# Optimization experiments

Measured on AMD Instinct MI355X. Metric: run time of the kernel, lower is better.

The kernel has to match this reference:

```python
import jax, jax.numpy as jnp
import numpy as np

N_ITERS = 10
OMEGA = 10
W_HALF = 512          # hpm.W
D = 2 * W_HALF        # real-lifted signal dim
BATCH = 4096
P_PREV = 8
EPS = 1e-8


def hard_thr(x, omega=OMEGA):
    # x: [B, D]; keep the omega largest-|x| entries per row, zero the rest
    # (equivalent to torch scatter-zero of the D-omega smallest |x|)
    _, idx = jax.lax.top_k(jnp.abs(x), omega)            # [B, omega]
    rows = jnp.arange(x.shape[0])[:, None]
    mask = jnp.zeros_like(x).at[rows, idx].set(1.0)
    return x * mask


def _spectral_density(z):
    # z: [B, D] -> squared complex magnitude summed over batch, min-max normalized
    w = z.shape[1] // 2
    p = z[:, :w] ** 2 + z[:, w:] ** 2                    # [B, W] (sign flip of imag part cancels)
    mD = p.sum(0)                                        # [W]
    return (mD - mD.min()) / (mD.max() - mD.min() + EPS)


def setup_inputs() -> dict:
    key = jax.random.key(0)
    k0, k1, k2 = jax.random.split(key, 3)
    x = jax.random.normal(k0, (BATCH, D), jnp.float32)
    prev_windows = jax.random.normal(k1, (P_PREV, BATCH, D), jnp.float32)
    # learned dictionary (stand-in for the real-lifted partial Fourier matrix)
    W_d = jax.random.normal(k2, (1, D, D), jnp.float32) / np.sqrt(D).astype(np.float32)
    L = jnp.float32(5.0)                                 # hpm.L (fixed Lipschitz constant)
    S = jnp.eye(D, dtype=jnp.float32)[None] - (1.0 / L) * jnp.matmul(
        jnp.swapaxes(W_d, 1, 2), W_d)                    # [1, D, D]
    lambda2 = jnp.float32(1.0)
    return {"x": x, "prev_windows": prev_windows, "W_d": W_d, "S": S,
            "lambda2": lambda2, "L": L}


def reference(x, prev_windows, W_d, S, lambda2, L):
    Wd0 = W_d[0]                                         # [D, D]
    S0 = S[0]                                            # [D, D]
    w = D // 2

    # B = (1/L * W_d) @ x   (column-vector matvec as row GEMM)
    b = (x @ Wd0.T) / L                                  # [B, D]

    # two warm-up ISTA/IHT steps
    z = hard_thr(b)
    c = b + z @ S0.T
    z = hard_thr(c)

    mD_normalized = _spectral_density(z)                 # [W]

    # ---- attention over previous windows (prev_windows non-empty branch) ----
    pw = prev_windows                                    # [P, B, D]
    p_prev = pw[:, :, :w] ** 2 + pw[:, :, w:] ** 2       # [P, B, W]
    mD_prev = p_prev.sum(1)                              # [P, W]
    mn = mD_prev.min(axis=1, keepdims=True)
    mx = mD_prev.max(axis=1, keepdims=True)
    prev_mDn = (mD_prev - mn) / (mx - mn + EPS)          # [P, W]

    att = prev_mDn @ mD_normalized[:, None]              # [P, 1]
    att = jax.nn.softmax(att / np.sqrt(float(w)).astype(np.float32), axis=0)
    pw_clamped = jnp.clip(pw, -150.0, 150.0)
    z = (pw_clamped * att[:, None]).sum(0) * lambda2     # [B, D]

    # ---- unrolled iterations ----
    for _ in range(N_ITERS):
        c = b + z @ S0.T
        z = hard_thr(c)

    mD_normalized = _spectral_density(z)                 # [W]
    return (mD_normalized, z)
```

## Files before the change

kernel.cpp:

```cpp
#include <hip/hip_runtime.h>
#include <stdint.h>

#define BATCH 4096
#define DIM   1024
#define PPREV 8

__device__ __forceinline__ int wave_max_i32(int v) {
    #pragma unroll
    for (int m = 1; m < 64; m <<= 1) v = max(v, __shfl_xor(v, m));
    return v;
}
__device__ __forceinline__ int wave_min_i32(int v) {
    #pragma unroll
    for (int m = 1; m < 64; m <<= 1) v = min(v, __shfl_xor(v, m));
    return v;
}
__device__ __forceinline__ int lt_count(unsigned long long m) {
    return __builtin_amdgcn_mbcnt_hi((unsigned)(m >> 32),
           __builtin_amdgcn_mbcnt_lo((unsigned)m, 0));
}


__device__ __forceinline__ void top10_full(const int kin[16], int sgn, int lane,
                                           int wi[10], float wv[10]) {
    int k[16];
    #pragma unroll
    for (int s = 0; s < 16; ++s) k[s] = kin[s];
    #pragma unroll
    for (int r = 0; r < 10; ++r) {
        int lm = k[0]; int ls = 0;
        #pragma unroll
        for (int s = 1; s < 16; ++s) { if (k[s] > lm) { lm = k[s]; ls = s; } }
        int m = wave_max_i32(lm);
        int cj = (lm == m) ? ((lane << 4) | ls) : 4096;
        int jw = wave_min_i32(cj);
        int wl = jw >> 4, ws = jw & 15;
        int sg = __shfl(sgn, wl);
        wi[r] = jw;
        wv[r] = __int_as_float(m | (((sg >> ws) & 1) << 31));
        if (lane == wl) {
            #pragma unroll
            for (int s = 0; s < 16; ++s) if (s == ws) k[s] = 0;
        }
    }
}

template<bool SEEDED>
__device__ __forceinline__ void select10(const float cz[16], int lane,
                                         int* s_kb, int* s_pay,
                                         int& tbits, int wi[10], float wv[10]) {
    int k[16]; int sgn = 0;
    #pragma unroll
    for (int s = 0; s < 16; ++s) {
        int bb = __float_as_int(cz[s]);
        k[s] = bb & 0x7fffffff;
        sgn |= (int)(((unsigned)bb >> 31) << s);
    }

    if (!SEEDED) {
        int lm = k[0];
        #pragma unroll
        for (int s = 1; s < 16; ++s) lm = max(lm, k[s]);
        #pragma unroll
        for (int k2 = 2; k2 <= 64; k2 <<= 1) {
            #pragma unroll
            for (int j = k2 >> 1; j > 0; j >>= 1) {
                int p = __shfl_xor(lm, j);
                bool keep_max = (((lane & k2) == 0) == ((lane & j) == 0));
                if ((p > lm) == keep_max) lm = p;
            }
        }
        tbits = __builtin_amdgcn_readlane(lm, 9);
    }

    int tb = tbits;
    int total;
    #pragma unroll 1
    for (;;) {
        total = 0;
        #pragma unroll
        for (int s = 0; s < 16; ++s)
            total += __popcll(__ballot(k[s] >= tb));
        if (total >= 10) break;
        tb = (tb > 0x00800000) ? (tb - 0x00800000) : 0;
    }

    if (total <= 64) {
        int base = 0;
        #pragma unroll
        for (int s = 0; s < 16; ++s) {
            unsigned long long bs = __ballot(k[s] >= tb);
            if (k[s] >= tb) {
                int pos = base + lt_count(bs);
                s_kb[pos]  = k[s];
                s_pay[pos] = ((1023 - ((lane << 4) | s)) << 1) | ((sgn >> s) & 1);
            }
            base += __popcll(bs);
        }
        asm volatile("s_waitcnt lgkmcnt(0)" ::: "memory");
        int kb = -1, pay = 0;
        if (lane < total) { kb = s_kb[lane]; pay = s_pay[lane]; }
        #pragma unroll
        for (int k2 = 2; k2 <= 64; k2 <<= 1) {
            #pragma unroll
            for (int j = k2 >> 1; j > 0; j >>= 1) {
                int pk = __shfl_xor(kb, j);
                int pp = __shfl_xor(pay, j);
                bool keep_max = (((lane & k2) == 0) == ((lane & j) == 0));
                bool gt = (pk > kb) || ((pk == kb) && (pp > pay));
                if (gt == keep_max) { kb = pk; pay = pp; }
            }
        }
        #pragma unroll
        for (int r = 0; r < 10; ++r) {
            int kr = __builtin_amdgcn_readlane(kb, r);
            int pr = __builtin_amdgcn_readlane(pay, r);
            wi[r] = 1023 - (pr >> 1);
            wv[r] = __int_as_float(kr | ((pr & 1) << 31));
        }
        tbits = __builtin_amdgcn_readlane(kb, 9);
    } else {
        top10_full(k, sgn, lane, wi, wv);
        tbits = __float_as_int(wv[9]) & 0x7fffffff;
    }
}

__device__ __forceinline__ void gather_ista(const float bz[16], float cz[16],
                                            const float* __restrict__ S,
                                            const int wi[10], const float wv[10], int lane) {
    #pragma unroll
    for (int s = 0; s < 16; ++s) cz[s] = bz[s];
    #pragma unroll
    for (int kk = 0; kk < 10; ++kk) {
        const float4* sp = (const float4*)(S + (size_t)wi[kk] * DIM + (lane << 4));
        const float wvs = wv[kk];
        #pragma unroll
        for (int q = 0; q < 4; ++q) {
            float4 v = sp[q];
            cz[q*4+0] += wvs * v.x;
            cz[q*4+1] += wvs * v.y;
            cz[q*4+2] += wvs * v.z;
            cz[q*4+3] += wvs * v.w;
        }
    }
}

__global__ __launch_bounds__(64)
void warmup_rows(const float* __restrict__ b, const float* __restrict__ S,
                 int* __restrict__ sidx, float* __restrict__ sval) {
    __shared__ int s_kb[64];
    __shared__ int s_pay[64];
    const int lane = threadIdx.x;
    const int r = blockIdx.x;
    const float* bp = b + (size_t)r * DIM + (lane << 4);
    float bz[16];
    #pragma unroll
    for (int q = 0; q < 4; ++q) {
        float4 v = ((const float4*)bp)[q];
        bz[q*4+0] = v.x; bz[q*4+1] = v.y; bz[q*4+2] = v.z; bz[q*4+3] = v.w;
    }
    int wi[10]; float wv[10]; int tbits = 0;
    select10<false>(bz, lane, s_kb, s_pay, tbits, wi, wv);
    float cz[16];
    gather_ista(bz, cz, S, wi, wv, lane);
    select10<true>(cz, lane, s_kb, s_pay, tbits, wi, wv);
    if (lane == 0) {
        #pragma unroll
        for (int kk = 0; kk < 10; ++kk) { sidx[r*10+kk] = wi[kk]; sval[r*10+kk] = wv[kk]; }
    }
}

__global__ __launch_bounds__(64)
void loop_rows(const float* __restrict__ c1, const float* __restrict__ b,
               const float* __restrict__ S, float* __restrict__ zout,
               int* __restrict__ sidx, float* __restrict__ sval) {
    __shared__ int s_kb[64];
    __shared__ int s_pay[64];
    const int lane = threadIdx.x;
    const int r = blockIdx.x;
    const float* bp = b  + (size_t)r * DIM + (lane << 4);
    const float* cp = c1 + (size_t)r * DIM + (lane << 4);
    float bz[16], cz[16];
    #pragma unroll
    for (int q = 0; q < 4; ++q) {
        float4 v = ((const float4*)bp)[q];
        bz[q*4+0] = v.x; bz[q*4+1] = v.y; bz[q*4+2] = v.z; bz[q*4+3] = v.w;
        float4 u = ((const float4*)cp)[q];
        cz[q*4+0] = u.x; cz[q*4+1] = u.y; cz[q*4+2] = u.z; cz[q*4+3] = u.w;
    }
    int wi[10]; float wv[10]; int tbits = 0;
    select10<false>(cz, lane, s_kb, s_pay, tbits, wi, wv);
    int pwi[10], pwb[10];
    #pragma unroll 1
    for (int it = 0; it < 9; ++it) {
        #pragma unroll
        for (int kk = 0; kk < 10; ++kk) { pwi[kk] = wi[kk]; pwb[kk] = __float_as_int(wv[kk]); }
        gather_ista(bz, cz, S, wi, wv, lane);
        select10<true>(cz, lane, s_kb, s_pay, tbits, wi, wv);
        bool same = true;
        #pragma unroll
        for (int kk = 0; kk < 10; ++kk)
            same = same && (wi[kk] == pwi[kk]) && (__float_as_int(wv[kk]) == pwb[kk]);
        if (same) break;
    }
    #pragma unroll
    for (int q = 0; q < 4; ++q) {
        float e[4];
        #pragma unroll
        for (int t = 0; t < 4; ++t) {
            int j = (lane << 4) | (q*4 + t);
            float v = 0.0f;
            #pragma unroll
            for (int kk = 0; kk < 10; ++kk) v = (wi[kk] == j) ? wv[kk] : v;
            e[t] = v;
        }
        float4 o; o.x = e[0]; o.y = e[1]; o.z = e[2]; o.w = e[3];
        ((float4*)(zout + (size_t)r * DIM + (lane << 4)))[q] = o;
    }
    if (lane == 0) {
        #pragma unroll
        for (int kk = 0; kk < 10; ++kk) { sidx[r*10+kk] = wi[kk]; sval[r*10+kk] = wv[kk]; }
    }
}

template<bool DIV_L, bool HAS_ADD>
__global__ __launch_bounds__(512)
void gemm128(const float* __restrict__ A, const float* __restrict__ B,
             const float* __restrict__ addM, float* __restrict__ C,
             const float* __restrict__ Lptr, int M, int N, int K) {
    __shared__ float As[16][132];
    __shared__ float Bs[16][132];
    const int tid = threadIdx.x;
    const int m0 = blockIdx.y * 128, n0 = blockIdx.x * 128;
    const int tx = tid & 15;
    const int ty = tid >> 4;
    const int srow = tid >> 2;
    const int sk   = (tid & 3) * 4;
    float acc[4][8] = {};
    const float* Ab = A + (size_t)(m0 + srow) * K + sk;
    const float* Bb = B + (size_t)(n0 + srow) * K + sk;
    for (int k0 = 0; k0 < K; k0 += 16) {
        float4 av = *(const float4*)(Ab + k0);
        float4 bv = *(const float4*)(Bb + k0);
        __syncthreads();
        As[sk+0][srow] = av.x; As[sk+1][srow] = av.y; As[sk+2][srow] = av.z; As[sk+3][srow] = av.w;
        Bs[sk+0][srow] = bv.x; Bs[sk+1][srow] = bv.y; Bs[sk+2][srow] = bv.z; Bs[sk+3][srow] = bv.w;
        __syncthreads();
        #pragma unroll
        for (int k = 0; k < 16; ++k) {
            float4 a4  = *(const float4*)&As[k][ty*4];
            float4 b40 = *(const float4*)&Bs[k][tx*8];
            float4 b41 = *(const float4*)&Bs[k][tx*8+4];
            float am[4] = {a4.x, a4.y, a4.z, a4.w};
            float bn[8] = {b40.x, b40.y, b40.z, b40.w, b41.x, b41.y, b41.z, b41.w};
            #pragma unroll
            for (int i = 0; i < 4; ++i)
                #pragma unroll
                for (int j = 0; j < 8; ++j)
                    acc[i][j] += am[i] * bn[j];
        }
    }
    const float invL = DIV_L ? (1.0f / *Lptr) : 1.0f;
    #pragma unroll
    for (int i = 0; i < 4; ++i) {
        size_t row = (size_t)(m0 + ty*4 + i);
        float* Cp = C + row * N + n0 + tx*8;
        #pragma unroll
        for (int j = 0; j < 8; ++j) {
            float r = acc[i][j];
            if (DIV_L) r *= invL;
            if (HAS_ADD) r += addM[row * N + n0 + tx*8 + j];
            Cp[j] = r;
        }
    }
}

__global__ void sparse_density_stage1(const int* __restrict__ sidx,
                                      const float* __restrict__ sval,
                                      float* __restrict__ partial) {
    const int w = threadIdx.x;
    const int blk = blockIdx.x;
    const int base = blk * 64 * 10;
    float acc = 0.0f;
    for (int e = 0; e < 640; ++e) {
        int d = sidx[base + e];
        float v = sval[base + e];
        if ((d & 511) == w) acc += v * v;
    }
    partial[blk * 512 + w] = acc;
}

__global__ void density_stage2(const float* __restrict__ partial, float* __restrict__ mD) {
    const int w = threadIdx.x;
    float acc = 0.0f;
    for (int i = 0; i < 64; ++i) acc += partial[i * 512 + w];
    mD[w] = acc;
}

__global__ void prev_density_stage1(const float* __restrict__ pw, float* __restrict__ partial) {
    const int p = blockIdx.x, chunk = blockIdx.y;
    const int w = threadIdx.x;
    const float* base = pw + ((size_t)p * BATCH + (size_t)chunk * 64) * DIM;
    float acc = 0.0f;
    for (int i = 0; i < 64; ++i) {
        float a = base[(size_t)i * DIM + w];
        float c = base[(size_t)i * DIM + 512 + w];
        acc += a * a + c * c;
    }
    partial[((size_t)(p * 64 + chunk)) * 512 + w] = acc;
}

__global__ void prev_density_stage2(const float* __restrict__ partial, float* __restrict__ mD_prev) {
    const int p = blockIdx.x; const int w = threadIdx.x;
    float acc = 0.0f;
    for (int i = 0; i < 64; ++i) acc += partial[((size_t)(p * 64 + i)) * 512 + w];
    mD_prev[p * 512 + w] = acc;
}

__device__ __forceinline__ float wave_fmax(float v) {
    #pragma unroll
    for (int m = 1; m < 64; m <<= 1) v = fmaxf(v, __shfl_xor(v, m));
    return v;
}
__device__ __forceinline__ float wave_fmin(float v) {
    #pragma unroll
    for (int m = 1; m < 64; m <<= 1) v = fminf(v, __shfl_xor(v, m));
    return v;
}
__device__ __forceinline__ float wave_fsum(float v) {
    #pragma unroll
    for (int m = 1; m < 64; m <<= 1) v += __shfl_xor(v, m);
    return v;
}

__global__ void attention_small(const float* __restrict__ mD1,
                                const float* __restrict__ mD_prev,
                                float* __restrict__ att) {
    __shared__ float att_l[PPREV];
    const int tid = threadIdx.x, lane = tid & 63, w = tid >> 6;
    float t8[8], u8[8];
    {
        const float4* m4 = (const float4*)(mD1 + lane * 8);
        float4 a = m4[0], bq = m4[1];
        t8[0]=a.x; t8[1]=a.y; t8[2]=a.z; t8[3]=a.w; t8[4]=bq.x; t8[5]=bq.y; t8[6]=bq.z; t8[7]=bq.w;
        const float4* p4 = (const float4*)(mD_prev + w * 512 + lane * 8);
        float4 c = p4[0], d = p4[1];
        u8[0]=c.x; u8[1]=c.y; u8[2]=c.z; u8[3]=c.w; u8[4]=d.x; u8[5]=d.y; u8[6]=d.z; u8[7]=d.w;
    }
    float mx = t8[0], mn = t8[0], pmx = u8[0], pmn = u8[0];
    #pragma unroll
    for (int i = 1; i < 8; ++i) {
        mx = fmaxf(mx, t8[i]); mn = fminf(mn, t8[i]);
        pmx = fmaxf(pmx, u8[i]); pmn = fminf(pmn, u8[i]);
    }
    mx = wave_fmax(mx); mn = wave_fmin(mn);
    pmx = wave_fmax(pmx); pmn = wave_fmin(pmn);
    const float inv  = 1.0f / (mx - mn + 1e-8f);
    const float pinv = 1.0f / (pmx - pmn + 1e-8f);
    float dot = 0.0f;
    #pragma unroll
    for (int i = 0; i < 8; ++i) dot += ((u8[i] - pmn) * pinv) * ((t8[i] - mn) * inv);
    dot = wave_fsum(dot);
    if (lane == 0) att_l[w] = dot / 22.627417f;
    __syncthreads();
    if (tid == 0) {
        float m = att_l[0];
        #pragma unroll
        for (int p = 1; p < PPREV; ++p) m = fmaxf(m, att_l[p]);
        float e[PPREV], s = 0.0f;
        #pragma unroll
        for (int p = 0; p < PPREV; ++p) { e[p] = expf(att_l[p] - m); s += e[p]; }
        #pragma unroll
        for (int p = 0; p < PPREV; ++p) att[p] = e[p] / s;
    }
}

__global__ __launch_bounds__(256)
void weighted_sum(const float* __restrict__ pw, const float* __restrict__ att,
                  const float* __restrict__ lam, float* __restrict__ zatt) {
    const size_t i = ((size_t)blockIdx.x * 256 + threadIdx.x) * 4;
    const float l2 = *lam;
    float a[PPREV];
    #pragma unroll
    for (int p = 0; p < PPREV; ++p) a[p] = att[p];
    float4 acc = make_float4(0.f, 0.f, 0.f, 0.f);
    #pragma unroll
    for (int p = 0; p < PPREV; ++p) {
        float4 v = *(const float4*)(pw + (size_t)p * BATCH * DIM + i);
        v.x = fminf(fmaxf(v.x, -150.f), 150.f);
        v.y = fminf(fmaxf(v.y, -150.f), 150.f);
        v.z = fminf(fmaxf(v.z, -150.f), 150.f);
        v.w = fminf(fmaxf(v.w, -150.f), 150.f);
        acc.x += v.x * a[p]; acc.y += v.y * a[p]; acc.z += v.z * a[p]; acc.w += v.w * a[p];
    }
    acc.x *= l2; acc.y *= l2; acc.z *= l2; acc.w *= l2;
    *(float4*)(zatt + i) = acc;
}

__global__ void finalize_fused(const float* __restrict__ partial, float* __restrict__ out) {
    __shared__ float red[512];
    const int tid = threadIdx.x;
    float v = 0.0f;
    for (int i = 0; i < 64; ++i) v += partial[i * 512 + tid];
    red[tid] = v; __syncthreads();
    for (int off = 256; off > 0; off >>= 1) { if (tid < off) red[tid] = fmaxf(red[tid], red[tid+off]); __syncthreads(); }
    float mx = red[0]; __syncthreads();
    red[tid] = v; __syncthreads();
    for (int off = 256; off > 0; off >>= 1) { if (tid < off) red[tid] = fminf(red[tid], red[tid+off]); __syncthreads(); }
    float mn = red[0];
    out[tid] = (v - mn) / (mx - mn + 1e-8f);
}

extern "C" void kernel_launch(void* const* d_in, const int* in_sizes, int n_in,
                              void* d_out, int out_size, void* d_ws, size_t ws_size,
                              hipStream_t stream) {
    const float* x   = (const float*)d_in[0];
    const float* pw  = (const float*)d_in[1];
    const float* Wd  = (const float*)d_in[2];
    const float* S   = (const float*)d_in[3];
    const float* lam = (const float*)d_in[4];
    const float* L   = (const float*)d_in[5];
    float* out = (float*)d_out;

    float* b       = (float*)d_ws;
    float* zatt    = b + (size_t)BATCH * DIM;
    float* pp_prev = zatt + (size_t)BATCH * DIM;
    float* pp_dens = pp_prev + 262144;
    float* mD1     = pp_dens + 32768;
    float* mD_prev = mD1 + 512;
    float* attw    = mD_prev + 4096;
    float* sval1   = attw + 8;
    float* sval2   = sval1 + 40960;
    int*   sidx1   = (int*)(sval2 + 40960);
    int*   sidx2   = sidx1 + 40960;

    float* c1   = out + 512;
    float* zout = out + 512;

    const dim3 gg(DIM / 128, BATCH / 128);

    gemm128<true,  false><<<gg, 512, 0, stream>>>(x, Wd, nullptr, b, L, BATCH, DIM, DIM);
    warmup_rows<<<BATCH, 64, 0, stream>>>(b, S, sidx1, sval1);
    sparse_density_stage1<<<64, 512, 0, stream>>>(sidx1, sval1, pp_dens);
    density_stage2<<<1, 512, 0, stream>>>(pp_dens, mD1);
    prev_density_stage1<<<dim3(PPREV, 64), 512, 0, stream>>>(pw, pp_prev);
    prev_density_stage2<<<PPREV, 512, 0, stream>>>(pp_prev, mD_prev);
    attention_small<<<1, 512, 0, stream>>>(mD1, mD_prev, attw);
    weighted_sum<<<(BATCH * DIM) / 1024, 256, 0, stream>>>(pw, attw, lam, zatt);
    gemm128<false, true ><<<gg, 512, 0, stream>>>(zatt, S, b, c1, nullptr, BATCH, DIM, DIM);
    loop_rows<<<BATCH, 64, 0, stream>>>(c1, b, S, zout, sidx2, sval2);
    sparse_density_stage1<<<64, 512, 0, stream>>>(sidx2, sval2, pp_dens);
    finalize_fused<<<1, 512, 0, stream>>>(pp_dens, out);
}
```

Before: 596.8 us.

## Rework top-10 selection, pack row kernels 4 waves/block, enlarge GEMM register tile

Several changes at once. The bitonic sort over candidates in select10 is replaced by a rank-counting selection through shared memory with packed int2 entries. The warmup and loop row kernels now run four rows per 256-thread block, and gather_ista uses readfirstlane so S row addresses are scalar. The GEMM drops to 256 threads with an 8x8 per-thread tile and register prefetch of the next K slab, and density_stage2 is fused into the attention kernel to remove one launch. The larger GEMM tile raises register pressure, and the rank loop is serial in the number of candidates.

```diff
diff --git a/kernel.cpp b/kernel.cpp
--- a/kernel.cpp
+++ b/kernel.cpp
@@ -47,7 +47,7 @@
 
 template<bool SEEDED>
 __device__ __forceinline__ void select10(const float cz[16], int lane,
-                                         int* s_kb, int* s_pay,
+                                         int2* s_cand, int2* s_win,
                                          int& tbits, int wi[10], float wv[10]) {
     int k[16]; int sgn = 0;
     #pragma unroll
@@ -92,33 +92,37 @@
             unsigned long long bs = __ballot(k[s] >= tb);
             if (k[s] >= tb) {
                 int pos = base + lt_count(bs);
-                s_kb[pos]  = k[s];
-                s_pay[pos] = ((1023 - ((lane << 4) | s)) << 1) | ((sgn >> s) & 1);
+                s_cand[pos] = make_int2(k[s], ((1023 - ((lane << 4) | s)) << 1) | ((sgn >> s) & 1));
             }
             base += __popcll(bs);
         }
         asm volatile("s_waitcnt lgkmcnt(0)" ::: "memory");
         int kb = -1, pay = 0;
-        if (lane < total) { kb = s_kb[lane]; pay = s_pay[lane]; }
-        #pragma unroll
-        for (int k2 = 2; k2 <= 64; k2 <<= 1) {
-            #pragma unroll
-            for (int j = k2 >> 1; j > 0; j >>= 1) {
-                int pk = __shfl_xor(kb, j);
-                int pp = __shfl_xor(pay, j);
-                bool keep_max = (((lane & k2) == 0) == ((lane & j) == 0));
-                bool gt = (pk > kb) || ((pk == kb) && (pp > pay));
-                if (gt == keep_max) { kb = pk; pay = pp; }
-            }
-        }
+        if (lane < total) { int2 c = s_cand[lane]; kb = c.x; pay = c.y; }
+        int rank = 0;
+        int e = 0;
+        #pragma unroll 1
+        for (; e + 4 <= total; e += 4) {
+            int2 c0 = s_cand[e], c1 = s_cand[e+1], c2 = s_cand[e+2], c3 = s_cand[e+3];
+            rank += ((c0.x > kb) || (c0.x == kb && c0.y > pay)) ? 1 : 0;
+            rank += ((c1.x > kb) || (c1.x == kb && c1.y > pay)) ? 1 : 0;
+            rank += ((c2.x > kb) || (c2.x == kb && c2.y > pay)) ? 1 : 0;
+            rank += ((c3.x > kb) || (c3.x == kb && c3.y > pay)) ? 1 : 0;
+        }
+        #pragma unroll 1
+        for (; e < total; ++e) {
+            int2 c = s_cand[e];
+            rank += ((c.x > kb) || (c.x == kb && c.y > pay)) ? 1 : 0;
+        }
+        if (lane < total && rank < 10) s_win[rank] = make_int2(kb, pay);
+        asm volatile("s_waitcnt lgkmcnt(0)" ::: "memory");
         #pragma unroll
         for (int r = 0; r < 10; ++r) {
-            int kr = __builtin_amdgcn_readlane(kb, r);
-            int pr = __builtin_amdgcn_readlane(pay, r);
-            wi[r] = 1023 - (pr >> 1);
-            wv[r] = __int_as_float(kr | ((pr & 1) << 31));
-        }
-        tbits = __builtin_amdgcn_readlane(kb, 9);
+            int2 wr = s_win[r];
+            wi[r] = 1023 - (wr.y >> 1);
+            wv[r] = __int_as_float(wr.x | ((wr.y & 1) << 31));
+        }
+        tbits = __float_as_int(wv[9]) & 0x7fffffff;
     } else {
         top10_full(k, sgn, lane, wi, wv);
         tbits = __float_as_int(wv[9]) & 0x7fffffff;
@@ -132,7 +136,8 @@
     for (int s = 0; s < 16; ++s) cz[s] = bz[s];
     #pragma unroll
     for (int kk = 0; kk < 10; ++kk) {
-        const float4* sp = (const float4*)(S + (size_t)wi[kk] * DIM + (lane << 4));
+        int row = __builtin_amdgcn_readfirstlane(wi[kk]);
+        const float4* sp = (const float4*)(S + (size_t)row * DIM + (lane << 4));
         const float wvs = wv[kk];
         #pragma unroll
         for (int q = 0; q < 4; ++q) {
@@ -145,13 +150,13 @@
     }
 }
 
-__global__ __launch_bounds__(64)
+__global__ __launch_bounds__(256)
 void warmup_rows(const float* __restrict__ b, const float* __restrict__ S,
                  int* __restrict__ sidx, float* __restrict__ sval) {
-    __shared__ int s_kb[64];
-    __shared__ int s_pay[64];
-    const int lane = threadIdx.x;
-    const int r = blockIdx.x;
+    __shared__ int2 s_cand[4][64];
+    __shared__ int2 s_win[4][16];
+    const int tid = threadIdx.x, lane = tid & 63, wid = tid >> 6;
+    const int r = blockIdx.x * 4 + wid;
     const float* bp = b + (size_t)r * DIM + (lane << 4);
     float bz[16];
     #pragma unroll
@@ -160,24 +165,24 @@
         bz[q*4+0] = v.x; bz[q*4+1] = v.y; bz[q*4+2] = v.z; bz[q*4+3] = v.w;
     }
     int wi[10]; float wv[10]; int tbits = 0;
-    select10<false>(bz, lane, s_kb, s_pay, tbits, wi, wv);
+    select10<false>(bz, lane, s_cand[wid], s_win[wid], tbits, wi, wv);
     float cz[16];
     gather_ista(bz, cz, S, wi, wv, lane);
-    select10<true>(cz, lane, s_kb, s_pay, tbits, wi, wv);
+    select10<true>(cz, lane, s_cand[wid], s_win[wid], tbits, wi, wv);
     if (lane == 0) {
         #pragma unroll
         for (int kk = 0; kk < 10; ++kk) { sidx[r*10+kk] = wi[kk]; sval[r*10+kk] = wv[kk]; }
     }
 }
 
-__global__ __launch_bounds__(64)
+__global__ __launch_bounds__(256)
 void loop_rows(const float* __restrict__ c1, const float* __restrict__ b,
                const float* __restrict__ S, float* __restrict__ zout,
                int* __restrict__ sidx, float* __restrict__ sval) {
-    __shared__ int s_kb[64];
-    __shared__ int s_pay[64];
-    const int lane = threadIdx.x;
-    const int r = blockIdx.x;
+    __shared__ int2 s_cand[4][64];
+    __shared__ int2 s_win[4][16];
+    const int tid = threadIdx.x, lane = tid & 63, wid = tid >> 6;
+    const int r = blockIdx.x * 4 + wid;
     const float* bp = b  + (size_t)r * DIM + (lane << 4);
     const float* cp = c1 + (size_t)r * DIM + (lane << 4);
     float bz[16], cz[16];
@@ -189,14 +194,14 @@
         cz[q*4+0] = u.x; cz[q*4+1] = u.y; cz[q*4+2] = u.z; cz[q*4+3] = u.w;
     }
     int wi[10]; float wv[10]; int tbits = 0;
-    select10<false>(cz, lane, s_kb, s_pay, tbits, wi, wv);
+    select10<false>(cz, lane, s_cand[wid], s_win[wid], tbits, wi, wv);
     int pwi[10], pwb[10];
     #pragma unroll 1
     for (int it = 0; it < 9; ++it) {
         #pragma unroll
         for (int kk = 0; kk < 10; ++kk) { pwi[kk] = wi[kk]; pwb[kk] = __float_as_int(wv[kk]); }
         gather_ista(bz, cz, S, wi, wv, lane);
-        select10<true>(cz, lane, s_kb, s_pay, tbits, wi, wv);
+        select10<true>(cz, lane, s_cand[wid], s_win[wid], tbits, wi, wv);
         bool same = true;
         #pragma unroll
         for (int kk = 0; kk < 10; ++kk)
@@ -224,37 +229,47 @@
 }
 
 template<bool DIV_L, bool HAS_ADD>
-__global__ __launch_bounds__(512)
-void gemm128(const float* __restrict__ A, const float* __restrict__ B,
+__global__ __launch_bounds__(256)
+void gemm256(const float* __restrict__ A, const float* __restrict__ B,
              const float* __restrict__ addM, float* __restrict__ C,
              const float* __restrict__ Lptr, int M, int N, int K) {
-    __shared__ float As[16][132];
-    __shared__ float Bs[16][132];
+    __shared__ float As[16][136];
+    __shared__ float Bs[16][136];
     const int tid = threadIdx.x;
     const int m0 = blockIdx.y * 128, n0 = blockIdx.x * 128;
-    const int tx = tid & 15;
-    const int ty = tid >> 4;
-    const int srow = tid >> 2;
-    const int sk   = (tid & 3) * 4;
-    float acc[4][8] = {};
+    const int ty = tid >> 4, tx = tid & 15;
+    const int srow = tid >> 1;
+    const int sk   = (tid & 1) * 8;
+    float acc[8][8] = {};
     const float* Ab = A + (size_t)(m0 + srow) * K + sk;
     const float* Bb = B + (size_t)(n0 + srow) * K + sk;
+    float4 av0 = *(const float4*)(Ab);
+    float4 av1 = *(const float4*)(Ab + 4);
+    float4 bv0 = *(const float4*)(Bb);
+    float4 bv1 = *(const float4*)(Bb + 4);
     for (int k0 = 0; k0 < K; k0 += 16) {
-        float4 av = *(const float4*)(Ab + k0);
-        float4 bv = *(const float4*)(Bb + k0);
         __syncthreads();
-        As[sk+0][srow] = av.x; As[sk+1][srow] = av.y; As[sk+2][srow] = av.z; As[sk+3][srow] = av.w;
-        Bs[sk+0][srow] = bv.x; Bs[sk+1][srow] = bv.y; Bs[sk+2][srow] = bv.z; Bs[sk+3][srow] = bv.w;
+        As[sk+0][srow] = av0.x; As[sk+1][srow] = av0.y; As[sk+2][srow] = av0.z; As[sk+3][srow] = av0.w;
+        As[sk+4][srow] = av1.x; As[sk+5][srow] = av1.y; As[sk+6][srow] = av1.z; As[sk+7][srow] = av1.w;
+        Bs[sk+0][srow] = bv0.x; Bs[sk+1][srow] = bv0.y; Bs[sk+2][srow] = bv0.z; Bs[sk+3][srow] = bv0.w;
+        Bs[sk+4][srow] = bv1.x; Bs[sk+5][srow] = bv1.y; Bs[sk+6][srow] = bv1.z; Bs[sk+7][srow] = bv1.w;
         __syncthreads();
+        if (k0 + 16 < K) {
+            av0 = *(const float4*)(Ab + k0 + 16);
+            av1 = *(const float4*)(Ab + k0 + 20);
+            bv0 = *(const float4*)(Bb + k0 + 16);
+            bv1 = *(const float4*)(Bb + k0 + 20);
+        }
         #pragma unroll
         for (int k = 0; k < 16; ++k) {
-            float4 a4  = *(const float4*)&As[k][ty*4];
+            float4 a40 = *(const float4*)&As[k][ty*8];
+            float4 a41 = *(const float4*)&As[k][ty*8+4];
             float4 b40 = *(const float4*)&Bs[k][tx*8];
             float4 b41 = *(const float4*)&Bs[k][tx*8+4];
-            float am[4] = {a4.x, a4.y, a4.z, a4.w};
-            float bn[8] = {b40.x, b40.y, b40.z, b40.w, b41.x, b41.y, b41.z, b41.w};
+            float am[8] = {a40.x,a40.y,a40.z,a40.w,a41.x,a41.y,a41.z,a41.w};
+            float bn[8] = {b40.x,b40.y,b40.z,b40.w,b41.x,b41.y,b41.z,b41.w};
             #pragma unroll
-            for (int i = 0; i < 4; ++i)
+            for (int i = 0; i < 8; ++i)
                 #pragma unroll
                 for (int j = 0; j < 8; ++j)
                     acc[i][j] += am[i] * bn[j];
@@ -262,14 +277,15 @@
     }
     const float invL = DIV_L ? (1.0f / *Lptr) : 1.0f;
     #pragma unroll
-    for (int i = 0; i < 4; ++i) {
-        size_t row = (size_t)(m0 + ty*4 + i);
+    for (int i = 0; i < 8; ++i) {
+        size_t row = (size_t)(m0 + ty*8 + i);
         float* Cp = C + row * N + n0 + tx*8;
+        const float* Ap = HAS_ADD ? (addM + row * N + n0 + tx*8) : nullptr;
         #pragma unroll
         for (int j = 0; j < 8; ++j) {
             float r = acc[i][j];
             if (DIV_L) r *= invL;
-            if (HAS_ADD) r += addM[row * N + n0 + tx*8 + j];
+            if (HAS_ADD) r += Ap[j];
             Cp[j] = r;
         }
     }
@@ -290,13 +306,6 @@
     partial[blk * 512 + w] = acc;
 }
 
-__global__ void density_stage2(const float* __restrict__ partial, float* __restrict__ mD) {
-    const int w = threadIdx.x;
-    float acc = 0.0f;
-    for (int i = 0; i < 64; ++i) acc += partial[i * 512 + w];
-    mD[w] = acc;
-}
-
 __global__ void prev_density_stage1(const float* __restrict__ pw, float* __restrict__ partial) {
     const int p = blockIdx.x, chunk = blockIdx.y;
     const int w = threadIdx.x;
@@ -333,14 +342,19 @@
     return v;
 }
 
-__global__ void attention_small(const float* __restrict__ mD1,
-                                const float* __restrict__ mD_prev,
-                                float* __restrict__ att) {
+__global__ void density2_attention(const float* __restrict__ partial,
+                                   const float* __restrict__ mD_prev,
+                                   float* __restrict__ att) {
+    __shared__ float md1[512];
     __shared__ float att_l[PPREV];
     const int tid = threadIdx.x, lane = tid & 63, w = tid >> 6;
+    float v = 0.0f;
+    for (int i = 0; i < 64; ++i) v += partial[i * 512 + tid];
+    md1[tid] = v;
+    __syncthreads();
     float t8[8], u8[8];
     {
-        const float4* m4 = (const float4*)(mD1 + lane * 8);
+        const float4* m4 = (const float4*)(&md1[lane * 8]);
         float4 a = m4[0], bq = m4[1];
         t8[0]=a.x; t8[1]=a.y; t8[2]=a.z; t8[3]=a.w; t8[4]=bq.x; t8[5]=bq.y; t8[6]=bq.z; t8[7]=bq.w;
         const float4* p4 = (const float4*)(mD_prev + w * 512 + lane * 8);
@@ -426,8 +440,7 @@
     float* zatt    = b + (size_t)BATCH * DIM;
     float* pp_prev = zatt + (size_t)BATCH * DIM;
     float* pp_dens = pp_prev + 262144;
-    float* mD1     = pp_dens + 32768;
-    float* mD_prev = mD1 + 512;
+    float* mD_prev = pp_dens + 32768;
     float* attw    = mD_prev + 4096;
     float* sval1   = attw + 8;
     float* sval2   = sval1 + 40960;
@@ -439,16 +452,15 @@
 
     const dim3 gg(DIM / 128, BATCH / 128);
 
-    gemm128<true,  false><<<gg, 512, 0, stream>>>(x, Wd, nullptr, b, L, BATCH, DIM, DIM);
-    warmup_rows<<<BATCH, 64, 0, stream>>>(b, S, sidx1, sval1);
+    gemm256<true,  false><<<gg, 256, 0, stream>>>(x, Wd, nullptr, b, L, BATCH, DIM, DIM);
+    warmup_rows<<<BATCH / 4, 256, 0, stream>>>(b, S, sidx1, sval1);
     sparse_density_stage1<<<64, 512, 0, stream>>>(sidx1, sval1, pp_dens);
-    density_stage2<<<1, 512, 0, stream>>>(pp_dens, mD1);
     prev_density_stage1<<<dim3(PPREV, 64), 512, 0, stream>>>(pw, pp_prev);
     prev_density_stage2<<<PPREV, 512, 0, stream>>>(pp_prev, mD_prev);
-    attention_small<<<1, 512, 0, stream>>>(mD1, mD_prev, attw);
+    density2_attention<<<1, 512, 0, stream>>>(pp_dens, mD_prev, attw);
     weighted_sum<<<(BATCH * DIM) / 1024, 256, 0, stream>>>(pw, attw, lam, zatt);
-    gemm128<false, true ><<<gg, 512, 0, stream>>>(zatt, S, b, c1, nullptr, BATCH, DIM, DIM);
-    loop_rows<<<BATCH, 64, 0, stream>>>(c1, b, S, zout, sidx2, sval2);
+    gemm256<false, true ><<<gg, 256, 0, stream>>>(zatt, S, b, c1, nullptr, BATCH, DIM, DIM);
+    loop_rows<<<BATCH / 4, 256, 0, stream>>>(c1, b, S, zout, sidx2, sval2);
     sparse_density_stage1<<<64, 512, 0, stream>>>(sidx2, sval2, pp_dens);
     finalize_fused<<<1, 512, 0, stream>>>(pp_dens, out);
 }
```

Result: slower. 610.6 us (+2.3%).
